# Performance work log

Hardware: AMD Instinct MI355X
Metric: run time of the kernel (lower is better)

Reference implementation:

```python
import jax, jax.numpy as jnp
import numpy as np


def setup_inputs() -> dict:
    key = jax.random.key(0)
    k1, k2, k3 = jax.random.split(key, 3)
    B, S, D = 2, 2048, 1024
    N_COMPRESS, RANK = 64, 64
    x = jax.random.normal(k1, (B, S, D), dtype=jnp.float32)
    router_w = jax.random.normal(k2, (N_COMPRESS, D), dtype=jnp.float32) * (1.0 / np.sqrt(D))
    # compress neurons (orthogonal-init in torch; gaussian scaled is fine for a numeric baseline)
    neurons = jax.random.normal(k3, (N_COMPRESS, D, RANK), dtype=jnp.float32) * (1.0 / np.sqrt(D))
    return {"x": x, "router_w": router_w, "neurons": neurons}


TOP_K = 2


def reference(x, router_w, neurons):
    # x: [B,S,D], router_w: [N,D], neurons: [N,D,R]
    B, S, D = x.shape
    R = neurons.shape[-1]
    scores = jnp.einsum('bsd,nd->bsn', x, router_w)            # [B,S,N]
    topk_scores, topk_idx = jax.lax.top_k(scores, TOP_K)       # [B,S,K]
    topk_weights = jax.nn.softmax(topk_scores, axis=-1)        # [B,S,K]
    output = jnp.zeros((B, S, R), dtype=x.dtype)
    for i in range(TOP_K):  # small fixed loop, mirrors original slot-wise combine
        idx = topk_idx[:, :, i]                                # [B,S]
        sel = neurons[idx]                                     # [B,S,D,R] gather
        proj = jnp.einsum('bsd,bsdr->bsr', x, sel)             # per-token matvec
        output = output + topk_weights[:, :, i:i + 1] * proj
    return output, topk_idx, topk_weights
```

## Files before the change

kernel.cpp:

```cpp
#include <hip/hip_runtime.h>
#include <hip/hip_bf16.h>


typedef unsigned short u16;
typedef unsigned int u32;
typedef __attribute__((ext_vector_type(8))) short short8;
typedef __attribute__((ext_vector_type(4))) float f32x4;

__device__ __forceinline__ float bf2f(u16 u) {
    u32 v = ((u32)u) << 16; float f; __builtin_memcpy(&f, &v, 4); return f;
}
__device__ __forceinline__ u16 f2bf(float f) {
    u32 u; __builtin_memcpy(&u, &f, 4);
    u32 r = u + 0x7fff + ((u >> 16) & 1);
    return (u16)(r >> 16);
}
__device__ __forceinline__ u32 pack2(float a, float b) {
    return ((u32)f2bf(b) << 16) | (u32)f2bf(a);
}

#define T_TOKENS 4096
#define DDIM 1024
#define NEXP 64
#define RDIM 64
#define LCAP 1024
#define OUT_IDX_OFF 262144
#define OUT_W_OFF 270336

struct LdBF {
    const u16* p;
    __device__ __forceinline__ float4 ld4(size_t i) const {
        ushort4 v = *(const ushort4*)(p + i);
        return make_float4(bf2f(v.x), bf2f(v.y), bf2f(v.z), bf2f(v.w));
    }
    __device__ __forceinline__ float ld1(size_t i) const { return bf2f(p[i]); }
};
struct LdF32 {
    const float* p;
    __device__ __forceinline__ float4 ld4(size_t i) const { return *(const float4*)(p + i); }
    __device__ __forceinline__ float ld1(size_t i) const { return p[i]; }
};

__device__ __forceinline__ int detect_f32(const u16* x, int* lds_cnt) {
    if (threadIdx.x == 0) *lds_cnt = 0;
    __syncthreads();
    if (threadIdx.x < 256) {
        unsigned e = (x[threadIdx.x] >> 7) & 0xFF;
        if (e >= 0x68 && e <= 0x88) atomicAdd(lds_cnt, 1);
    }
    __syncthreads();
    int f = (*lds_cnt < 200) ? 1 : 0;
    __syncthreads();
    return f;
}

template <class LD>
__device__ __forceinline__ void score_body(LD xld, LD rwld,
                                           float* xs , float* wt ,
                                           float* sc ,
                                           float* out, float* wsW,
                                           int* wsCnt, int* wsList) {
    const int tid = threadIdx.x;
    const size_t t0 = (size_t)blockIdx.x * 8;
    const int wv = tid >> 6;
    const int lane = tid & 63;
    const int tg = lane & 1;
    const int eg = (lane >> 1) & 7;
    const int kql = (lane >> 4) & 3;
    const int dd = 4 * kql + 16 * wv;
    const int kc0 = blockIdx.x & 15;

    if (tid < 128) {
        float4 z = make_float4(0.f, 0.f, 0.f, 0.f);
        ((float4*)out)[(size_t)blockIdx.x * 128 + tid] = z;
    }

    const int sm = tid >> 4;
    const int sd4 = (tid & 15) * 4;

    float acc[4][8];
#pragma unroll
    for (int mi = 0; mi < 4; ++mi)
#pragma unroll
        for (int ei = 0; ei < 8; ++ei) acc[mi][ei] = 0.f;

    float4 px;
    if (tid < 128) px = xld.ld4((t0 + sm) * DDIM + kc0 * 64 + sd4);
    float4 pw[4];
#pragma unroll
    for (int h = 0; h < 4; ++h) {
        int i4 = tid + h * 256;
        pw[h] = rwld.ld4((size_t)(i4 >> 4) * DDIM + kc0 * 64 + (i4 & 15) * 4);
    }

    for (int i = 0; i < 16; ++i) {
        if (i > 0) __syncthreads();
        if (tid < 128) *(float4*)&xs[sm * 68 + sd4] = px;
#pragma unroll
        for (int h = 0; h < 4; ++h) {
            int i4 = tid + h * 256;
            *(float4*)&wt[(i4 >> 4) * 68 + (i4 & 15) * 4] = pw[h];
        }
        __syncthreads();

        if (i < 15) {
            int kn = ((i + 1 + kc0) & 15) * 64;
            if (tid < 128) px = xld.ld4((t0 + sm) * DDIM + kn + sd4);
#pragma unroll
            for (int h = 0; h < 4; ++h) {
                int i4 = tid + h * 256;
                pw[h] = rwld.ld4((size_t)(i4 >> 4) * DDIM + kn + (i4 & 15) * 4);
            }
        }

        float4 xv[4], wv4[8];
#pragma unroll
        for (int mi = 0; mi < 4; ++mi)
            xv[mi] = *(const float4*)&xs[(tg + 2 * mi) * 68 + dd];
#pragma unroll
        for (int ei = 0; ei < 8; ++ei)
            wv4[ei] = *(const float4*)&wt[(eg + 8 * ei) * 68 + dd];
#pragma unroll
        for (int mi = 0; mi < 4; ++mi)
#pragma unroll
            for (int ei = 0; ei < 8; ++ei)
                acc[mi][ei] += xv[mi].x * wv4[ei].x + xv[mi].y * wv4[ei].y +
                               xv[mi].z * wv4[ei].z + xv[mi].w * wv4[ei].w;
    }

#pragma unroll
    for (int mi = 0; mi < 4; ++mi)
#pragma unroll
        for (int ei = 0; ei < 8; ++ei) {
            float v = acc[mi][ei];
            v += __shfl_xor(v, 16, 64);
            v += __shfl_xor(v, 32, 64);
            acc[mi][ei] = v;
        }
    __syncthreads();

    for (int w = 0; w < 4; ++w) {
        if (wv == w && kql == 0) {
#pragma unroll
            for (int mi = 0; mi < 4; ++mi)
#pragma unroll
                for (int ei = 0; ei < 8; ++ei) {
                    int idx = (tg + 2 * mi) * 65 + eg + 8 * ei;
                    sc[idx] = (w == 0) ? acc[mi][ei] : sc[idx] + acc[mi][ei];
                }
        }
        __syncthreads();
    }

    if (tid < 8) {
        const float* s = &sc[tid * 65];
        float best = -1e30f, secv = -1e30f;
        int bi = 0, si = 0;
        for (int j = 0; j < NEXP; ++j) {
            float v = s[j];
            if (v > best) { secv = best; si = bi; best = v; bi = j; }
            else if (v > secv) { secv = v; si = j; }
        }
        float w0 = 1.0f / (1.0f + expf(secv - best));
        float w1 = 1.0f - w0;
        size_t t = t0 + tid;
        out[OUT_IDX_OFF + t * 2 + 0] = (float)bi;
        out[OUT_IDX_OFF + t * 2 + 1] = (float)si;
        out[OUT_W_OFF + t * 2 + 0] = w0;
        out[OUT_W_OFF + t * 2 + 1] = w1;
        wsW[t * 2 + 0] = w0;
        wsW[t * 2 + 1] = w1;
        int p0 = atomicAdd(&wsCnt[bi], 1);
        if (p0 < LCAP) wsList[bi * LCAP + p0] = (int)(t * 2 + 0);
        int p1 = atomicAdd(&wsCnt[si], 1);
        if (p1 < LCAP) wsList[si * LCAP + p1] = (int)(t * 2 + 1);
    }
}

__global__ __launch_bounds__(256, 2) void score_topk(const void* x, const void* rw,
                                                     float* out, float* wsW,
                                                     int* wsCnt, int* wsList) {
    __shared__ float xs[8 * 68];
    __shared__ float wt[64 * 68];
    __shared__ float sc[8 * 65];
    __shared__ int dc;
    int f = detect_f32((const u16*)x, &dc);
    if (f)
        score_body(LdF32{(const float*)x}, LdF32{(const float*)rw}, xs, wt, sc, out, wsW, wsCnt, wsList);
    else
        score_body(LdBF{(const u16*)x}, LdBF{(const u16*)rw}, xs, wt, sc, out, wsW, wsCnt, wsList);
}

template <class LD>
__device__ __forceinline__ void egemm_body(LD xld, LD nld,
                                           const int* wsCnt, const int* wsList,
                                           const float* wsW, float* out,
                                           u16* Ab , u16* Bb ,
                                           int* entL ) {
    const int tid = threadIdx.x;
    const int e = blockIdx.x & 63;
    const int ti = blockIdx.x >> 6;
    const int cntE = min(wsCnt[e], LCAP);
    const int base = ti * 16;
    if (base >= cntE) return;
    const int valid = min(16, cntE - base);
    const int wv = tid >> 6;
    const int lane = tid & 63;
    const int l15 = lane & 15, quad = lane >> 4;
    const size_t nbase = (size_t)e * (DDIM * RDIM);

    if (tid < 16)
        entL[tid] = wsList[e * LCAP + base + min(tid, valid - 1)];
    __syncthreads();

    f32x4 acc = {0.f, 0.f, 0.f, 0.f};

    for (int kc = 0; kc < 8; ++kc) {
        const int k0c = kc * 128;
        if (kc > 0) __syncthreads();
#pragma unroll
        for (int h = 0; h < 16; ++h) {
            int p = tid + h * 256;
            int r = p & 63, kp = p >> 6;
            float g0 = nld.ld1(nbase + (size_t)(k0c + 2 * kp) * RDIM + r);
            float g1 = nld.ld1(nbase + (size_t)(k0c + 2 * kp + 1) * RDIM + r);
            ((u32*)Bb)[r * 68 + kp] = pack2(g0, g1);
        }
#pragma unroll
        for (int h = 0; h < 4; ++h) {
            int p = tid + h * 256;
            int row = p >> 6, kp = p & 63;
            size_t tt = (size_t)(entL[row] >> 1);
            float g0 = xld.ld1(tt * DDIM + k0c + 2 * kp);
            float g1 = xld.ld1(tt * DDIM + k0c + 2 * kp + 1);
            ((u32*)Ab)[row * 68 + kp] = pack2(g0, g1);
        }
        __syncthreads();

#pragma unroll
        for (int ko = 0; ko < 4; ++ko) {
            int kofs = ko * 32 + quad * 8;
            short8 bfr = *(const short8*)&Bb[(16 * wv + l15) * 136 + kofs];
            short8 af = *(const short8*)&Ab[l15 * 136 + kofs];
            acc = __builtin_amdgcn_mfma_f32_16x16x32_bf16(af, bfr, acc, 0, 0, 0);
        }
    }

#pragma unroll
    for (int reg = 0; reg < 4; ++reg) {
        int m = quad * 4 + reg;
        if (m < valid) {
            int t2 = entL[m];
            atomicAdd(&out[(size_t)(t2 >> 1) * RDIM + 16 * wv + l15], wsW[t2] * acc[reg]);
        }
    }
}

__global__ __launch_bounds__(256) void expert_gemm(const void* x, const void* neurons,
                                                   const int* wsCnt, const int* wsList,
                                                   const float* wsW, float* out) {
    __shared__ u16 Ab[16 * 136];
    __shared__ u16 Bb[64 * 136];
    __shared__ int entL[16];
    __shared__ int dc;
    int f = detect_f32((const u16*)x, &dc);
    if (f)
        egemm_body(LdF32{(const float*)x}, LdF32{(const float*)neurons}, wsCnt, wsList, wsW, out, Ab, Bb, entL);
    else
        egemm_body(LdBF{(const u16*)x}, LdBF{(const u16*)neurons}, wsCnt, wsList, wsW, out, Ab, Bb, entL);
}

extern "C" void kernel_launch(void* const* d_in, const int* in_sizes, int n_in,
                              void* d_out, int out_size, void* d_ws, size_t ws_size,
                              hipStream_t stream) {
    const void* x = d_in[0];
    const void* rw = d_in[1];
    const void* neurons = d_in[2];
    float* out = (float*)d_out;

    char* wsc = (char*)d_ws;
    float* wsW = (float*)wsc;
    int* wsCnt = (int*)(wsc + 32 * 1024);
    int* wsList = (int*)((char*)wsCnt + 256);

    hipMemsetAsync(wsCnt, 0, 256, stream);
    score_topk<<<512, 256, 0, stream>>>(x, rw, out, wsW, wsCnt, wsList);
    expert_gemm<<<1024, 256, 0, stream>>>(x, neurons, wsCnt, wsList, wsW, out);
}
```

Before: 128.5 us.

## Halve score tokens per block and vectorize register-prefetched expert GEMM tile loads

The scoring kernel now handles 4 tokens per block instead of 8 and launches twice as many blocks with a higher occupancy hint, so more CUs are busy on the router GEMV. The expert GEMM replaces scalar per-element global loads with float4 loads held in registers, prefetching the next K-chunk while the current one is packed into LDS and computed. This is meant to cut load-instruction count and memory latency stalls. In exchange it uses more registers per thread and reloads router weights twice as often in the scoring pass.

```diff
diff --git a/kernel.cpp b/kernel.cpp
--- a/kernel.cpp
+++ b/kernel.cpp
@@ -61,31 +61,31 @@
                                            float* out, float* wsW,
                                            int* wsCnt, int* wsList) {
     const int tid = threadIdx.x;
-    const size_t t0 = (size_t)blockIdx.x * 8;
+    const size_t t0 = (size_t)blockIdx.x * 4;
     const int wv = tid >> 6;
     const int lane = tid & 63;
     const int tg = lane & 1;
     const int eg = (lane >> 1) & 7;
     const int kql = (lane >> 4) & 3;
-    const int dd = 4 * kql + 16 * wv;
+    const int dd = 16 * kql + 4 * wv;
     const int kc0 = blockIdx.x & 15;
 
-    if (tid < 128) {
+    if (tid < 64) {
         float4 z = make_float4(0.f, 0.f, 0.f, 0.f);
-        ((float4*)out)[(size_t)blockIdx.x * 128 + tid] = z;
-    }
-
-    const int sm = tid >> 4;
+        ((float4*)out)[(size_t)blockIdx.x * 64 + tid] = z;
+    }
+
+    const int sm = (tid >> 4) & 3;
     const int sd4 = (tid & 15) * 4;
 
-    float acc[4][8];
-#pragma unroll
-    for (int mi = 0; mi < 4; ++mi)
+    float acc[2][8];
+#pragma unroll
+    for (int mi = 0; mi < 2; ++mi)
 #pragma unroll
         for (int ei = 0; ei < 8; ++ei) acc[mi][ei] = 0.f;
 
     float4 px;
-    if (tid < 128) px = xld.ld4((t0 + sm) * DDIM + kc0 * 64 + sd4);
+    if (tid < 64) px = xld.ld4((t0 + sm) * DDIM + kc0 * 64 + sd4);
     float4 pw[4];
 #pragma unroll
     for (int h = 0; h < 4; ++h) {
@@ -95,7 +95,7 @@
 
     for (int i = 0; i < 16; ++i) {
         if (i > 0) __syncthreads();
-        if (tid < 128) *(float4*)&xs[sm * 68 + sd4] = px;
+        if (tid < 64) *(float4*)&xs[sm * 68 + sd4] = px;
 #pragma unroll
         for (int h = 0; h < 4; ++h) {
             int i4 = tid + h * 256;
@@ -105,7 +105,7 @@
 
         if (i < 15) {
             int kn = ((i + 1 + kc0) & 15) * 64;
-            if (tid < 128) px = xld.ld4((t0 + sm) * DDIM + kn + sd4);
+            if (tid < 64) px = xld.ld4((t0 + sm) * DDIM + kn + sd4);
 #pragma unroll
             for (int h = 0; h < 4; ++h) {
                 int i4 = tid + h * 256;
@@ -113,15 +113,15 @@
             }
         }
 
-        float4 xv[4], wv4[8];
-#pragma unroll
-        for (int mi = 0; mi < 4; ++mi)
+        float4 xv[2], wv4[8];
+#pragma unroll
+        for (int mi = 0; mi < 2; ++mi)
             xv[mi] = *(const float4*)&xs[(tg + 2 * mi) * 68 + dd];
 #pragma unroll
         for (int ei = 0; ei < 8; ++ei)
             wv4[ei] = *(const float4*)&wt[(eg + 8 * ei) * 68 + dd];
 #pragma unroll
-        for (int mi = 0; mi < 4; ++mi)
+        for (int mi = 0; mi < 2; ++mi)
 #pragma unroll
             for (int ei = 0; ei < 8; ++ei)
                 acc[mi][ei] += xv[mi].x * wv4[ei].x + xv[mi].y * wv4[ei].y +
@@ -129,7 +129,7 @@
     }
 
 #pragma unroll
-    for (int mi = 0; mi < 4; ++mi)
+    for (int mi = 0; mi < 2; ++mi)
 #pragma unroll
         for (int ei = 0; ei < 8; ++ei) {
             float v = acc[mi][ei];
@@ -142,7 +142,7 @@
     for (int w = 0; w < 4; ++w) {
         if (wv == w && kql == 0) {
 #pragma unroll
-            for (int mi = 0; mi < 4; ++mi)
+            for (int mi = 0; mi < 2; ++mi)
 #pragma unroll
                 for (int ei = 0; ei < 8; ++ei) {
                     int idx = (tg + 2 * mi) * 65 + eg + 8 * ei;
@@ -152,7 +152,7 @@
         __syncthreads();
     }
 
-    if (tid < 8) {
+    if (tid < 4) {
         const float* s = &sc[tid * 65];
         float best = -1e30f, secv = -1e30f;
         int bi = 0, si = 0;
@@ -177,12 +177,12 @@
     }
 }
 
-__global__ __launch_bounds__(256, 2) void score_topk(const void* x, const void* rw,
+__global__ __launch_bounds__(256, 4) void score_topk(const void* x, const void* rw,
                                                      float* out, float* wsW,
                                                      int* wsCnt, int* wsList) {
-    __shared__ float xs[8 * 68];
+    __shared__ float xs[4 * 68];
     __shared__ float wt[64 * 68];
-    __shared__ float sc[8 * 65];
+    __shared__ float sc[4 * 65];
     __shared__ int dc;
     int f = detect_f32((const u16*)x, &dc);
     if (f)
@@ -213,28 +213,47 @@
         entL[tid] = wsList[e * LCAP + base + min(tid, valid - 1)];
     __syncthreads();
 
+    const int rq = tid & 15;
+    const int kpB = tid >> 4;
+    const int rowA = tid >> 4;
+    const int kqA = tid & 15;
+    const size_t xrow = (size_t)(entL[rowA] >> 1) * DDIM;
+
+    float4 bg0[4], bg1[4], ag0, ag1;
+    auto LOADC = [&](int k0c) {
+#pragma unroll
+        for (int h = 0; h < 4; ++h) {
+            int kp = kpB + h * 16;
+            bg0[h] = nld.ld4(nbase + (size_t)(k0c + 2 * kp) * RDIM + rq * 4);
+            bg1[h] = nld.ld4(nbase + (size_t)(k0c + 2 * kp + 1) * RDIM + rq * 4);
+        }
+        ag0 = xld.ld4(xrow + k0c + kqA * 8);
+        ag1 = xld.ld4(xrow + k0c + kqA * 8 + 4);
+    };
+
     f32x4 acc = {0.f, 0.f, 0.f, 0.f};
+    LOADC(0);
 
     for (int kc = 0; kc < 8; ++kc) {
-        const int k0c = kc * 128;
         if (kc > 0) __syncthreads();
-#pragma unroll
-        for (int h = 0; h < 16; ++h) {
-            int p = tid + h * 256;
-            int r = p & 63, kp = p >> 6;
-            float g0 = nld.ld1(nbase + (size_t)(k0c + 2 * kp) * RDIM + r);
-            float g1 = nld.ld1(nbase + (size_t)(k0c + 2 * kp + 1) * RDIM + r);
-            ((u32*)Bb)[r * 68 + kp] = pack2(g0, g1);
-        }
+        u32* bb = (u32*)Bb;
 #pragma unroll
         for (int h = 0; h < 4; ++h) {
-            int p = tid + h * 256;
-            int row = p >> 6, kp = p & 63;
-            size_t tt = (size_t)(entL[row] >> 1);
-            float g0 = xld.ld1(tt * DDIM + k0c + 2 * kp);
-            float g1 = xld.ld1(tt * DDIM + k0c + 2 * kp + 1);
-            ((u32*)Ab)[row * 68 + kp] = pack2(g0, g1);
-        }
+            int kp = kpB + h * 16;
+            bb[(rq * 4 + 0) * 68 + kp] = pack2(bg0[h].x, bg1[h].x);
+            bb[(rq * 4 + 1) * 68 + kp] = pack2(bg0[h].y, bg1[h].y);
+            bb[(rq * 4 + 2) * 68 + kp] = pack2(bg0[h].z, bg1[h].z);
+            bb[(rq * 4 + 3) * 68 + kp] = pack2(bg0[h].w, bg1[h].w);
+        }
+        {
+            uint4 w;
+            w.x = pack2(ag0.x, ag0.y);
+            w.y = pack2(ag0.z, ag0.w);
+            w.z = pack2(ag1.x, ag1.y);
+            w.w = pack2(ag1.z, ag1.w);
+            *(uint4*)&((u32*)Ab)[rowA * 68 + kqA * 4] = w;
+        }
+        if (kc < 7) LOADC((kc + 1) * 128);
         __syncthreads();
 
 #pragma unroll
@@ -256,9 +275,9 @@
     }
 }
 
-__global__ __launch_bounds__(256) void expert_gemm(const void* x, const void* neurons,
-                                                   const int* wsCnt, const int* wsList,
-                                                   const float* wsW, float* out) {
+__global__ __launch_bounds__(256, 2) void expert_gemm(const void* x, const void* neurons,
+                                                      const int* wsCnt, const int* wsList,
+                                                      const float* wsW, float* out) {
     __shared__ u16 Ab[16 * 136];
     __shared__ u16 Bb[64 * 136];
     __shared__ int entL[16];
@@ -284,6 +303,6 @@
     int* wsList = (int*)((char*)wsCnt + 256);
 
     hipMemsetAsync(wsCnt, 0, 256, stream);
-    score_topk<<<512, 256, 0, stream>>>(x, rw, out, wsW, wsCnt, wsList);
+    score_topk<<<1024, 256, 0, stream>>>(x, rw, out, wsW, wsCnt, wsList);
     expert_gemm<<<1024, 256, 0, stream>>>(x, neurons, wsCnt, wsList, wsW, out);
 }
```

New measurement: 140.4 us. 1.09x slower.

## Keep expert weights resident in LDS and loop over token tiles per block

Applied to the files above, without the earlier changes.

Expert GEMM now launches one block per (expert, K-half), stages that half of the expert's weights into shared memory once, and iterates over all token tiles for that expert. Global loads are vectorized to float4. This removes repeated weight reloads across token-tile blocks. In exchange it cuts the grid to 128 blocks with serialized tile loops and larger LDS use, which reduces parallelism and is sensitive to routing imbalance. It also doubles the output atomics because of the K split.

```diff
diff --git a/kernel.cpp b/kernel.cpp
--- a/kernel.cpp
+++ b/kernel.cpp
@@ -198,69 +198,88 @@
                                            u16* Ab , u16* Bb ,
                                            int* entL ) {
     const int tid = threadIdx.x;
-    const int e = blockIdx.x & 63;
-    const int ti = blockIdx.x >> 6;
+    const int e = blockIdx.x >> 1;
+    const int kh = blockIdx.x & 1;
     const int cntE = min(wsCnt[e], LCAP);
-    const int base = ti * 16;
-    if (base >= cntE) return;
-    const int valid = min(16, cntE - base);
+    if (cntE <= 0) return;
     const int wv = tid >> 6;
     const int lane = tid & 63;
     const int l15 = lane & 15, quad = lane >> 4;
     const size_t nbase = (size_t)e * (DDIM * RDIM);
 
-    if (tid < 16)
-        entL[tid] = wsList[e * LCAP + base + min(tid, valid - 1)];
-    __syncthreads();
-
-    f32x4 acc = {0.f, 0.f, 0.f, 0.f};
-
-    for (int kc = 0; kc < 8; ++kc) {
-        const int k0c = kc * 128;
-        if (kc > 0) __syncthreads();
-#pragma unroll
-        for (int h = 0; h < 16; ++h) {
-            int p = tid + h * 256;
-            int r = p & 63, kp = p >> 6;
-            float g0 = nld.ld1(nbase + (size_t)(k0c + 2 * kp) * RDIM + r);
-            float g1 = nld.ld1(nbase + (size_t)(k0c + 2 * kp + 1) * RDIM + r);
-            ((u32*)Bb)[r * 68 + kp] = pack2(g0, g1);
-        }
+    const int rq = tid & 15;
+    const int kpB = tid >> 4;
+    for (int s = 0; s < 4; ++s) {
+        u32* bb = (u32*)Bb + s * (64 * 68);
+        const int k0c = kh * 512 + s * 128;
 #pragma unroll
         for (int h = 0; h < 4; ++h) {
-            int p = tid + h * 256;
-            int row = p >> 6, kp = p & 63;
-            size_t tt = (size_t)(entL[row] >> 1);
-            float g0 = xld.ld1(tt * DDIM + k0c + 2 * kp);
-            float g1 = xld.ld1(tt * DDIM + k0c + 2 * kp + 1);
-            ((u32*)Ab)[row * 68 + kp] = pack2(g0, g1);
-        }
-        __syncthreads();
-
-#pragma unroll
-        for (int ko = 0; ko < 4; ++ko) {
-            int kofs = ko * 32 + quad * 8;
-            short8 bfr = *(const short8*)&Bb[(16 * wv + l15) * 136 + kofs];
-            short8 af = *(const short8*)&Ab[l15 * 136 + kofs];
-            acc = __builtin_amdgcn_mfma_f32_16x16x32_bf16(af, bfr, acc, 0, 0, 0);
-        }
-    }
-
-#pragma unroll
-    for (int reg = 0; reg < 4; ++reg) {
-        int m = quad * 4 + reg;
-        if (m < valid) {
-            int t2 = entL[m];
-            atomicAdd(&out[(size_t)(t2 >> 1) * RDIM + 16 * wv + l15], wsW[t2] * acc[reg]);
-        }
-    }
-}
-
-__global__ __launch_bounds__(256) void expert_gemm(const void* x, const void* neurons,
-                                                   const int* wsCnt, const int* wsList,
-                                                   const float* wsW, float* out) {
-    __shared__ u16 Ab[16 * 136];
-    __shared__ u16 Bb[64 * 136];
+            int kp = kpB + h * 16;
+            float4 g0 = nld.ld4(nbase + (size_t)(k0c + 2 * kp) * RDIM + rq * 4);
+            float4 g1 = nld.ld4(nbase + (size_t)(k0c + 2 * kp + 1) * RDIM + rq * 4);
+            bb[(rq * 4 + 0) * 68 + kp] = pack2(g0.x, g1.x);
+            bb[(rq * 4 + 1) * 68 + kp] = pack2(g0.y, g1.y);
+            bb[(rq * 4 + 2) * 68 + kp] = pack2(g0.z, g1.z);
+            bb[(rq * 4 + 3) * 68 + kp] = pack2(g0.w, g1.w);
+        }
+    }
+
+    const int rowA = tid >> 4;
+    const int kqA = tid & 15;
+
+    for (int ti = 0; ti * 16 < cntE; ++ti) {
+        const int base = ti * 16;
+        const int valid = min(16, cntE - base);
+        __syncthreads();
+        if (tid < 16)
+            entL[tid] = wsList[e * LCAP + base + min(tid, valid - 1)];
+        __syncthreads();
+        const size_t xrow = (size_t)(entL[rowA] >> 1) * DDIM + kh * 512;
+
+        float4 a0[4], a1[4];
+#pragma unroll
+        for (int kc = 0; kc < 4; ++kc) {
+            a0[kc] = xld.ld4(xrow + kc * 128 + kqA * 8);
+            a1[kc] = xld.ld4(xrow + kc * 128 + kqA * 8 + 4);
+        }
+#pragma unroll
+        for (int kc = 0; kc < 4; ++kc) {
+            uint4 w;
+            w.x = pack2(a0[kc].x, a0[kc].y);
+            w.y = pack2(a0[kc].z, a0[kc].w);
+            w.z = pack2(a1[kc].x, a1[kc].y);
+            w.w = pack2(a1[kc].z, a1[kc].w);
+            *(uint4*)&((u32*)Ab)[kc * (16 * 68) + rowA * 68 + kqA * 4] = w;
+        }
+        __syncthreads();
+
+        f32x4 acc = {0.f, 0.f, 0.f, 0.f};
+#pragma unroll
+        for (int kc = 0; kc < 4; ++kc)
+#pragma unroll
+            for (int ko = 0; ko < 4; ++ko) {
+                int kofs = ko * 32 + quad * 8;
+                short8 bfr = *(const short8*)&Bb[kc * (64 * 136) + (16 * wv + l15) * 136 + kofs];
+                short8 af = *(const short8*)&Ab[kc * (16 * 136) + l15 * 136 + kofs];
+                acc = __builtin_amdgcn_mfma_f32_16x16x32_bf16(af, bfr, acc, 0, 0, 0);
+            }
+
+#pragma unroll
+        for (int reg = 0; reg < 4; ++reg) {
+            int m = quad * 4 + reg;
+            if (m < valid) {
+                int t2 = entL[m];
+                atomicAdd(&out[(size_t)(t2 >> 1) * RDIM + 16 * wv + l15], wsW[t2] * acc[reg]);
+            }
+        }
+    }
+}
+
+__global__ __launch_bounds__(256, 1) void expert_gemm(const void* x, const void* neurons,
+                                                      const int* wsCnt, const int* wsList,
+                                                      const float* wsW, float* out) {
+    __shared__ u16 Ab[4 * 16 * 136];
+    __shared__ u16 Bb[4 * 64 * 136];
     __shared__ int entL[16];
     __shared__ int dc;
     int f = detect_f32((const u16*)x, &dc);
@@ -285,5 +304,5 @@
 
     hipMemsetAsync(wsCnt, 0, 256, stream);
     score_topk<<<512, 256, 0, stream>>>(x, rw, out, wsW, wsCnt, wsList);
-    expert_gemm<<<1024, 256, 0, stream>>>(x, neurons, wsCnt, wsList, wsW, out);
-}
+    expert_gemm<<<128, 256, 0, stream>>>(x, neurons, wsCnt, wsList, wsW, out);
+}
```

After: 145.9 us. +13.6%, slower.
